# Kernel optimization log

Hardware: AMD Instinct MI355X
Metric: run time of the kernel (lower is better)

## Reference

```python
import jax, jax.numpy as jnp
import numpy as np
import math

D_MODEL = 1024
N_HEAD = 16
B, S = 4, 2048


def setup_inputs() -> dict:
    key = jax.random.key(0)
    ks = jax.random.split(key, 9)
    sc = 1.0 / math.sqrt(D_MODEL)
    inp = {
        "x": jax.random.normal(ks[0], (B, S, D_MODEL), dtype=jnp.float32),
        "Wq": jax.random.normal(ks[1], (D_MODEL, D_MODEL), dtype=jnp.float32) * sc,
        "bq": jnp.zeros((D_MODEL,), dtype=jnp.float32),
        "Wk": jax.random.normal(ks[2], (D_MODEL, D_MODEL), dtype=jnp.float32) * sc,
        "bk": jnp.zeros((D_MODEL,), dtype=jnp.float32),
        "Wv": jax.random.normal(ks[3], (D_MODEL, D_MODEL), dtype=jnp.float32) * sc,
        "bv": jnp.zeros((D_MODEL,), dtype=jnp.float32),
        "Wo": jax.random.normal(ks[4], (D_MODEL, D_MODEL), dtype=jnp.float32) * sc,
        "bo": jnp.zeros((D_MODEL,), dtype=jnp.float32),
    }
    return inp


def _split_heads(t):
    # [b, s, h*d] -> [b, h, s, d]
    b, s, _ = t.shape
    return t.reshape(b, s, N_HEAD, D_MODEL // N_HEAD).transpose(0, 2, 1, 3)


def reference(x, Wq, bq, Wk, bk, Wv, bv, Wo, bo):
    b, s, d = x.shape
    d_k = d // N_HEAD
    q = _split_heads(x @ Wq.T + bq)
    k = _split_heads(x @ Wk.T + bk)
    v = _split_heads(x @ Wv.T + bv)
    # full score matrix [b, h, s, s] with causal tril mask
    scores = jnp.einsum('bhnd,bhmd->bhnm', q, k) / math.sqrt(d_k)
    causal = jnp.tril(jnp.ones((s, s), dtype=bool))
    scores = jnp.where(causal, scores, -jnp.inf)
    probs = jax.nn.softmax(scores, axis=-1)
    attn = jnp.einsum('bhnm,bhmd->bhnd', probs, v)
    attn = attn.transpose(0, 2, 1, 3).reshape(b, s, d)
    return attn @ Wo.T + bo
```

## Files before the change

kernel.cpp:

```cpp
#include <hip/hip_runtime.h>
#include <hip/hip_bf16.h>

#define D_MODEL 1024
#define N_HEADS 16
#define DK      64
#define BATCH   4
#define SEQ     2048
#define NROW    (BATCH*SEQ)

#define ASZ (256*64)
#define BSZ (128*64)

typedef __attribute__((ext_vector_type(8)))  short bf16x8;
typedef __attribute__((ext_vector_type(4)))  float f32x4;
typedef __attribute__((ext_vector_type(16))) float f32x16;
typedef __attribute__((ext_vector_type(4)))  unsigned int u32x4;

__device__ __forceinline__ unsigned short f2bf(float f) {
  unsigned int u = __float_as_uint(f);
  u += 0x7fff + ((u >> 16) & 1);
  return (unsigned short)(u >> 16);
}

__device__ __forceinline__ void gload_lds16(const void* g, void* l) {
  __builtin_amdgcn_global_load_lds((const __attribute__((address_space(1))) void*)g,
                                   (__attribute__((address_space(3))) void*)l,
                                   16, 0, 0);
}

__global__ void cvt_bf16(const float* __restrict__ s, unsigned short* __restrict__ d, int n4) {
  int i = blockIdx.x * 256 + threadIdx.x;
  if (i >= n4) return;
  float4 f = reinterpret_cast<const float4*>(s)[i];
  ushort4 o;
  o.x = f2bf(f.x); o.y = f2bf(f.y); o.z = f2bf(f.z); o.w = f2bf(f.w);
  reinterpret_cast<ushort4*>(d)[i] = o;
}

__global__ void cvt_bf16_w4(const float* __restrict__ s0, const float* __restrict__ s1,
                            const float* __restrict__ s2, const float* __restrict__ s3,
                            unsigned short* __restrict__ d0, unsigned short* __restrict__ d1,
                            unsigned short* __restrict__ d2, unsigned short* __restrict__ d3,
                            int n4) {
  int i = blockIdx.x * 256 + threadIdx.x;
  if (i >= n4) return;
  const float* s = blockIdx.z == 0 ? s0 : blockIdx.z == 1 ? s1 : blockIdx.z == 2 ? s2 : s3;
  unsigned short* d = blockIdx.z == 0 ? d0 : blockIdx.z == 1 ? d1 : blockIdx.z == 2 ? d2 : d3;
  float4 f = reinterpret_cast<const float4*>(s)[i];
  ushort4 o;
  o.x = f2bf(f.x); o.y = f2bf(f.y); o.z = f2bf(f.z); o.w = f2bf(f.w);
  reinterpret_cast<ushort4*>(d)[i] = o;
}

template<int OUT_MODE>
__device__ __forceinline__ void gemm_body(unsigned short* __restrict__ As,
                                          unsigned short* __restrict__ Bs,
                                          const unsigned short* __restrict__ A,
                                          const unsigned short* __restrict__ Bw,
                                          const float* __restrict__ bias,
                                          unsigned short* __restrict__ Cb,
                                          float* __restrict__ Cf, float scale)
{
  const int tid  = threadIdx.x;
  const int lane = tid & 63;
  const int w    = tid >> 6;
  const int wr   = w >> 2;
  const int wc   = w & 3;
  const int m0   = blockIdx.x * 256;
  const int n0   = blockIdx.y * 128;
  const int r    = lane & 15;
  const int ko   = (lane >> 4) * 8;
  const int xorA = (r & 7) << 3;
  const int srow = lane >> 3;
  const int scol = (((lane & 7) ^ ((lane >> 3) & 7)) << 3);

  f32x4 acc[8][2] = {};

  auto STAGE = [&](int buf, int kt) {
#pragma unroll
    for (int p = 0; p < 4; ++p) {
      int c = w * 4 + p;
      gload_lds16(A + (size_t)(m0 + c*8 + srow) * D_MODEL + kt + scol,
                  As + buf*ASZ + c*512);
    }
#pragma unroll
    for (int p = 0; p < 2; ++p) {
      int c = w * 2 + p;
      gload_lds16(Bw + (size_t)(n0 + c*8 + srow) * D_MODEL + kt + scol,
                  Bs + buf*BSZ + c*512);
    }
  };

  STAGE(0, 0);
  for (int it = 0; it < 16; ++it) {
    const int cur = it & 1;
    if (it < 15) {
      STAGE(cur ^ 1, (it + 1) * 64);
      asm volatile("s_waitcnt vmcnt(6)" ::: "memory");
    } else {
      asm volatile("s_waitcnt vmcnt(0)" ::: "memory");
    }
    __builtin_amdgcn_s_barrier();
    __builtin_amdgcn_sched_barrier(0);

    __builtin_amdgcn_s_setprio(1);
#pragma unroll
    for (int ks = 0; ks < 2; ++ks) {
      bf16x8 af[8], bfr[2];
#pragma unroll
      for (int m = 0; m < 8; ++m)
        af[m]  = *reinterpret_cast<const bf16x8*>(
            As + cur*ASZ + (wr*128 + m*16 + r)*64 + ((ks*32 + ko) ^ xorA));
#pragma unroll
      for (int n = 0; n < 2; ++n)
        bfr[n] = *reinterpret_cast<const bf16x8*>(
            Bs + cur*BSZ + (wc*32 + n*16 + r)*64 + ((ks*32 + ko) ^ xorA));
#pragma unroll
      for (int m = 0; m < 8; ++m)
#pragma unroll
        for (int n = 0; n < 2; ++n)
          acc[m][n] = __builtin_amdgcn_mfma_f32_16x16x32_bf16(af[m], bfr[n], acc[m][n], 0, 0, 0);
    }
    __builtin_amdgcn_s_setprio(0);
    __builtin_amdgcn_s_barrier();
  }

  const int rq = (lane >> 4) * 4;
#pragma unroll
  for (int m = 0; m < 8; ++m) {
#pragma unroll
    for (int n = 0; n < 2; ++n) {
      int col = n0 + wc*32 + n*16 + r;
      float bv = bias[col];
      int r0 = m0 + wr*128 + m*16 + rq;
      if (OUT_MODE == 2) {
        ushort4 o;
        o.x = f2bf(acc[m][n][0] + bv); o.y = f2bf(acc[m][n][1] + bv);
        o.z = f2bf(acc[m][n][2] + bv); o.w = f2bf(acc[m][n][3] + bv);
        size_t addr = (size_t)((r0 >> 11) * 1024 + col) * SEQ + (r0 & 2047);
        *reinterpret_cast<ushort4*>(Cb + addr) = o;
      } else {
#pragma unroll
        for (int i = 0; i < 4; ++i) {
          float v = (acc[m][n][i] + bv) * scale;
          if (OUT_MODE == 0) Cb[(size_t)(r0 + i) * D_MODEL + col] = f2bf(v);
          else               Cf[(size_t)(r0 + i) * D_MODEL + col] = v;
        }
      }
    }
  }
}

#define QSCALE (0.125f * 1.4426950408889634f)

__global__ __launch_bounds__(512, 2)
void gemm_qkv(const unsigned short* __restrict__ xb,
              const unsigned short* __restrict__ Wqb,
              const unsigned short* __restrict__ Wkb,
              const unsigned short* __restrict__ Wvb,
              const float* __restrict__ bq, const float* __restrict__ bk,
              const float* __restrict__ bv,
              unsigned short* __restrict__ Qb, unsigned short* __restrict__ Kb,
              unsigned short* __restrict__ Vt)
{
  __shared__ __align__(16) unsigned short smem[2*ASZ + 2*BSZ];
  unsigned short* As = smem;
  unsigned short* Bs = smem + 2*ASZ;
  if (blockIdx.z == 0)      gemm_body<0>(As, Bs, xb, Wqb, bq, Qb, nullptr, QSCALE);
  else if (blockIdx.z == 1) gemm_body<0>(As, Bs, xb, Wkb, bk, Kb, nullptr, 1.0f);
  else                      gemm_body<2>(As, Bs, xb, Wvb, bv, Vt, nullptr, 1.0f);
}

__global__ __launch_bounds__(512, 2)
void gemm_out(const unsigned short* __restrict__ Ab,
              const unsigned short* __restrict__ Wob,
              const float* __restrict__ bo, float* __restrict__ Cf)
{
  __shared__ __align__(16) unsigned short smem[2*ASZ + 2*BSZ];
  gemm_body<1>(smem, smem + 2*ASZ, Ab, Wob, bo, nullptr, Cf, 1.0f);
}

__global__ __launch_bounds__(256, 3)
void attn_fwd(const unsigned short* __restrict__ Qb,
              const unsigned short* __restrict__ Kb,
              const unsigned short* __restrict__ Vt,
              unsigned short* __restrict__ Ab)
{
  __shared__ __align__(16) unsigned short Ks[2][64*64];
  __shared__ __align__(16) unsigned short Vs[2][64*64];
  const int tid  = threadIdx.x;
  const int lane = tid & 63;
  const int w    = tid >> 6;
  const int flat = blockIdx.x;
  const int xcd  = flat & 7;
  const int idx  = flat >> 3;
  const int bh   = xcd * 8 + (idx & 7);
  const int qt   = 15 - (idx >> 3);
  const int b    = bh >> 4;
  const int h    = bh & 15;
  const size_t base = (size_t)b * SEQ;
  const int q0   = qt * 128;
  const int l31  = lane & 31;
  const int half = lane >> 5;
  const int aw   = q0 + w*32;
  const int qg   = aw + l31;
  const int nt   = (q0 + 127) >> 6;
  const int xorK = (l31 & 7) << 3;
  const int scolS = (((lane & 7) ^ ((lane >> 3) & 7)) << 3);
  const int srowS = lane >> 3;

  bf16x8 qf[4];
#pragma unroll
  for (int s = 0; s < 4; ++s)
    qf[s] = *reinterpret_cast<const bf16x8*>(
        Qb + (base + qg) * D_MODEL + h*DK + s*16 + half*8);

  f32x16 acc[2] = {};
  float mrun = -INFINITY, lrun = 0.f;

  auto STAGE = [&](int buf, int t) {
#pragma unroll
    for (int p = 0; p < 2; ++p) {
      int c = w*2 + p;
      gload_lds16(Kb + (base + t*64 + c*8 + srowS) * D_MODEL + h*DK + scolS, &Ks[buf][c*512]);
      gload_lds16(Vt + ((size_t)(b*1024 + h*DK) + c*8 + srowS) * SEQ + t*64 + scolS, &Vs[buf][c*512]);
    }
  };

  STAGE(0, 0);
  asm volatile("s_waitcnt vmcnt(0)" ::: "memory");

  for (int t = 0; t <= nt; ++t) {
    const int cur = t & 1;
    if (t < nt) {
      STAGE(cur ^ 1, t + 1);
      asm volatile("s_waitcnt vmcnt(4)" ::: "memory");
    } else {
      asm volatile("s_waitcnt vmcnt(0)" ::: "memory");
    }
    __builtin_amdgcn_s_barrier();
    __builtin_amdgcn_sched_barrier(0);

    const bool dead = (t << 6) > aw + 31;
    if (!dead) {
      f32x16 sacc[2] = {};
      __builtin_amdgcn_s_setprio(1);
#pragma unroll
      for (int kg = 0; kg < 2; ++kg)
#pragma unroll
        for (int s = 0; s < 4; ++s) {
          bf16x8 kf = *reinterpret_cast<const bf16x8*>(
              &Ks[cur][(kg*32 + l31)*64 + ((s*16 + half*8) ^ xorK)]);
          sacc[kg] = __builtin_amdgcn_mfma_f32_32x32x16_bf16(kf, qf[s], sacc[kg], 0, 0, 0);
        }
      __builtin_amdgcn_s_setprio(0);

      if ((t << 6) + 63 > aw) {
        const int kbase = (t << 6) + half*4;
#pragma unroll
        for (int kg = 0; kg < 2; ++kg)
#pragma unroll
          for (int g = 0; g < 16; ++g) {
            int k = kbase + kg*32 + (g & 3) + ((g >> 2) << 3);
            if (k > qg) sacc[kg][g] = -INFINITY;
          }
      }

      float tmax = sacc[0][0];
#pragma unroll
      for (int kg = 0; kg < 2; ++kg)
#pragma unroll
        for (int g = 0; g < 16; ++g) tmax = fmaxf(tmax, sacc[kg][g]);
      tmax = fmaxf(tmax, __shfl_xor(tmax, 32));

      if (__any(tmax > mrun + 8.0f)) {
        float nm = fmaxf(mrun, tmax);
        float fs = exp2f(mrun - nm);
        mrun = nm; lrun *= fs;
#pragma unroll
        for (int dg = 0; dg < 2; ++dg)
#pragma unroll
          for (int g = 0; g < 16; ++g) acc[dg][g] *= fs;
      }

      unsigned int pw[2][2][4];
#pragma unroll
      for (int kg = 0; kg < 2; ++kg) {
#pragma unroll
        for (int g = 0; g < 16; ++g) {
          float pv = exp2f(sacc[kg][g] - mrun);
          sacc[kg][g] = pv;
          lrun += pv;
        }
#pragma unroll
        for (int i = 0; i < 2; ++i) {
          unsigned int a, bb, c, d;
          asm("v_cvt_pk_bf16_f32 %0, %1, %2" : "=v"(a)  : "v"(sacc[kg][2*i]),    "v"(sacc[kg][2*i+1]));
          asm("v_cvt_pk_bf16_f32 %0, %1, %2" : "=v"(bb) : "v"(sacc[kg][4+2*i]),  "v"(sacc[kg][5+2*i]));
          asm("v_cvt_pk_bf16_f32 %0, %1, %2" : "=v"(c)  : "v"(sacc[kg][8+2*i]),  "v"(sacc[kg][9+2*i]));
          asm("v_cvt_pk_bf16_f32 %0, %1, %2" : "=v"(d)  : "v"(sacc[kg][12+2*i]), "v"(sacc[kg][13+2*i]));
          asm("v_permlane32_swap_b32 %0, %1" : "+v"(a), "+v"(bb));
          asm("v_permlane32_swap_b32 %0, %1" : "+v"(c), "+v"(d));
          pw[kg][0][i] = a; pw[kg][0][2+i] = bb;
          pw[kg][1][i] = c; pw[kg][1][2+i] = d;
        }
      }

      __builtin_amdgcn_s_setprio(1);
#pragma unroll
      for (int dg = 0; dg < 2; ++dg)
#pragma unroll
        for (int kg = 0; kg < 2; ++kg)
#pragma unroll
          for (int st = 0; st < 2; ++st) {
            int vrow = dg*32 + l31;
            int vcol = kg*32 + st*16 + half*8;
            bf16x8 vf = *reinterpret_cast<const bf16x8*>(
                &Vs[cur][vrow*64 + (vcol ^ xorK)]);
            bf16x8 pf = __builtin_bit_cast(bf16x8,
                u32x4{pw[kg][st][0], pw[kg][st][1], pw[kg][st][2], pw[kg][st][3]});
            acc[dg] = __builtin_amdgcn_mfma_f32_32x32x16_bf16(vf, pf, acc[dg], 0, 0, 0);
          }
      __builtin_amdgcn_s_setprio(0);
    }
    __builtin_amdgcn_s_barrier();
  }

  float ltot = lrun + __shfl_xor(lrun, 32);
  float rinv = 1.0f / ltot;
  unsigned short* Os = &Ks[0][0];
  const int qloc = w*32 + l31;
#pragma unroll
  for (int dg = 0; dg < 2; ++dg)
#pragma unroll
    for (int g = 0; g < 16; ++g) {
      int d = dg*32 + (g & 3) + ((g >> 2) << 3) + half*4;
      Os[qloc*64 + (d ^ ((qloc & 7) << 3))] = f2bf(acc[dg][g] * rinv);
    }
  __syncthreads();
  {
    const int q  = tid >> 1;
    const int c0 = (tid & 1) * 32;
#pragma unroll
    for (int u = 0; u < 4; ++u) {
      int c = c0 + u*8;
      bf16x8 vv = *reinterpret_cast<const bf16x8*>(&Os[q*64 + (c ^ ((q & 7) << 3))]);
      *reinterpret_cast<bf16x8*>(&Ab[(base + q0 + q) * D_MODEL + h*DK + c]) = vv;
    }
  }
}

extern "C" void kernel_launch(void* const* d_in, const int* in_sizes, int n_in,
                              void* d_out, int out_size, void* d_ws, size_t ws_size,
                              hipStream_t stream) {
  const float* x  = (const float*)d_in[0];
  const float* Wq = (const float*)d_in[1];
  const float* bq = (const float*)d_in[2];
  const float* Wk = (const float*)d_in[3];
  const float* bk = (const float*)d_in[4];
  const float* Wv = (const float*)d_in[5];
  const float* bv = (const float*)d_in[6];
  const float* Wo = (const float*)d_in[7];
  const float* bo = (const float*)d_in[8];

  unsigned short* ws = (unsigned short*)d_ws;
  const size_t NX = (size_t)NROW * D_MODEL;
  const size_t NW = (size_t)D_MODEL * D_MODEL;
  unsigned short* xb  = ws;
  unsigned short* Wqb = xb  + NX;
  unsigned short* Wkb = Wqb + NW;
  unsigned short* Wvb = Wkb + NW;
  unsigned short* Wob = Wvb + NW;
  unsigned short* Qb  = Wob + NW;
  unsigned short* Kb  = Qb  + NX;
  unsigned short* Vt  = Kb  + NX;
  unsigned short* Ab  = xb;

  cvt_bf16<<<dim3((unsigned)(NX/4/256)), 256, 0, stream>>>(x, xb, (int)(NX/4));
  cvt_bf16_w4<<<dim3((unsigned)(NW/4/256), 1, 4), 256, 0, stream>>>(
      Wq, Wk, Wv, Wo, Wqb, Wkb, Wvb, Wob, (int)(NW/4));

  gemm_qkv<<<dim3(NROW/256, D_MODEL/128, 3), 512, 0, stream>>>(
      xb, Wqb, Wkb, Wvb, bq, bk, bv, Qb, Kb, Vt);

  attn_fwd<<<dim3(1024), 256, 0, stream>>>(Qb, Kb, Vt, Ab);

  gemm_out<<<dim3(NROW/256, D_MODEL/128, 1), 512, 0, stream>>>(
      Ab, Wob, bo, (float*)d_out);
}
```

Measured before the change: 164.9 us.

## Compute softmax row sums via MFMA with ones, tree-reduce max, raise occupancy

The attention kernel now accumulates the softmax denominator with an extra MFMA that multiplies a ones vector by the bf16 probability tile. This replaces the per-element scalar adds and the final cross-half shuffle. The row max becomes a pairwise tree reduction to shorten the dependency chain. The epilogue packs two outputs per bf16 convert and does 32-bit LDS stores, and launch bounds move from 3 to 4 blocks per CU. In exchange it adds a 16-register accumulator and extra MFMA work, the sum now comes from bf16-rounded probabilities, and the tighter occupancy bound may cause register spills.

```diff
diff --git a/kernel.cpp b/kernel.cpp
--- a/kernel.cpp
+++ b/kernel.cpp
@@ -180,7 +180,7 @@
   gemm_body<1>(smem, smem + 2*ASZ, Ab, Wob, bo, nullptr, Cf, 1.0f);
 }
 
-__global__ __launch_bounds__(256, 3)
+__global__ __launch_bounds__(256, 4)
 void attn_fwd(const unsigned short* __restrict__ Qb,
               const unsigned short* __restrict__ Kb,
               const unsigned short* __restrict__ Vt,
@@ -215,8 +215,13 @@
     qf[s] = *reinterpret_cast<const bf16x8*>(
         Qb + (base + qg) * D_MODEL + h*DK + s*16 + half*8);
 
+  bf16x8 ones8;
+#pragma unroll
+  for (int i = 0; i < 8; ++i) ones8[i] = (short)0x3F80;
+
   f32x16 acc[2] = {};
-  float mrun = -INFINITY, lrun = 0.f;
+  f32x16 ssum = {};
+  float mrun = -INFINITY;
 
   auto STAGE = [&](int buf, int t) {
 #pragma unroll
@@ -266,17 +271,21 @@
           }
       }
 
-      float tmax = sacc[0][0];
-#pragma unroll
-      for (int kg = 0; kg < 2; ++kg)
-#pragma unroll
-        for (int g = 0; g < 16; ++g) tmax = fmaxf(tmax, sacc[kg][g]);
-      tmax = fmaxf(tmax, __shfl_xor(tmax, 32));
+      float tm[16];
+#pragma unroll
+      for (int g = 0; g < 16; ++g) tm[g] = fmaxf(sacc[0][g], sacc[1][g]);
+#pragma unroll
+      for (int s = 8; s > 0; s >>= 1)
+#pragma unroll
+        for (int g = 0; g < s; ++g) tm[g] = fmaxf(tm[g], tm[g + s]);
+      float tmax = fmaxf(tm[0], __shfl_xor(tm[0], 32));
 
       if (__any(tmax > mrun + 8.0f)) {
         float nm = fmaxf(mrun, tmax);
         float fs = exp2f(mrun - nm);
-        mrun = nm; lrun *= fs;
+        mrun = nm;
+#pragma unroll
+        for (int g = 0; g < 16; ++g) ssum[g] *= fs;
 #pragma unroll
         for (int dg = 0; dg < 2; ++dg)
 #pragma unroll
@@ -287,11 +296,8 @@
 #pragma unroll
       for (int kg = 0; kg < 2; ++kg) {
 #pragma unroll
-        for (int g = 0; g < 16; ++g) {
-          float pv = exp2f(sacc[kg][g] - mrun);
-          sacc[kg][g] = pv;
-          lrun += pv;
-        }
+        for (int g = 0; g < 16; ++g)
+          sacc[kg][g] = exp2f(sacc[kg][g] - mrun);
 #pragma unroll
         for (int i = 0; i < 2; ++i) {
           unsigned int a, bb, c, d;
@@ -308,35 +314,43 @@
 
       __builtin_amdgcn_s_setprio(1);
 #pragma unroll
-      for (int dg = 0; dg < 2; ++dg)
-#pragma unroll
-        for (int kg = 0; kg < 2; ++kg)
-#pragma unroll
-          for (int st = 0; st < 2; ++st) {
+      for (int kg = 0; kg < 2; ++kg)
+#pragma unroll
+        for (int st = 0; st < 2; ++st) {
+          bf16x8 pf = __builtin_bit_cast(bf16x8,
+              u32x4{pw[kg][st][0], pw[kg][st][1], pw[kg][st][2], pw[kg][st][3]});
+          ssum = __builtin_amdgcn_mfma_f32_32x32x16_bf16(ones8, pf, ssum, 0, 0, 0);
+#pragma unroll
+          for (int dg = 0; dg < 2; ++dg) {
             int vrow = dg*32 + l31;
             int vcol = kg*32 + st*16 + half*8;
             bf16x8 vf = *reinterpret_cast<const bf16x8*>(
                 &Vs[cur][vrow*64 + (vcol ^ xorK)]);
-            bf16x8 pf = __builtin_bit_cast(bf16x8,
-                u32x4{pw[kg][st][0], pw[kg][st][1], pw[kg][st][2], pw[kg][st][3]});
             acc[dg] = __builtin_amdgcn_mfma_f32_32x32x16_bf16(vf, pf, acc[dg], 0, 0, 0);
           }
+        }
       __builtin_amdgcn_s_setprio(0);
     }
     __builtin_amdgcn_s_barrier();
   }
 
-  float ltot = lrun + __shfl_xor(lrun, 32);
-  float rinv = 1.0f / ltot;
+  float rinv = 1.0f / ssum[0];
   unsigned short* Os = &Ks[0][0];
   const int qloc = w*32 + l31;
+  const int swzq = (qloc & 7) << 3;
 #pragma unroll
   for (int dg = 0; dg < 2; ++dg)
 #pragma unroll
-    for (int g = 0; g < 16; ++g) {
-      int d = dg*32 + (g & 3) + ((g >> 2) << 3) + half*4;
-      Os[qloc*64 + (d ^ ((qloc & 7) << 3))] = f2bf(acc[dg][g] * rinv);
-    }
+    for (int a = 0; a < 4; ++a)
+#pragma unroll
+      for (int p = 0; p < 2; ++p) {
+        int g0 = 4*a + 2*p;
+        int dd = dg*32 + 8*a + half*4 + 2*p;
+        unsigned int u;
+        float lo = acc[dg][g0] * rinv, hi = acc[dg][g0+1] * rinv;
+        asm("v_cvt_pk_bf16_f32 %0, %1, %2" : "=v"(u) : "v"(lo), "v"(hi));
+        *reinterpret_cast<unsigned int*>(&Os[qloc*64 + (dd ^ swzq)]) = u;
+      }
   __syncthreads();
   {
     const int q  = tid >> 1;
```

New measurement: 191.8 us. +16.3%, slower.
